# Kernel tuning notes

Measured on AMD Instinct MI355X. Metric: run time of the kernel, lower is better.

## Reference

```python
import jax, jax.numpy as jnp
import numpy as np

N, E, F_NODE, F_EDGE, H, EH, G = 20000, 200000, 32, 8, 256, 16, 512
OUT_DIMS = [H, H, H // 2]  # 256, 256, 128
BN_EPS = 1e-5


def _lin(k, out_c, in_c):
    kw, kb = jax.random.split(k)
    bound = 1.0 / np.sqrt(in_c)
    w = jax.random.uniform(kw, (out_c, in_c), minval=-bound, maxval=bound, dtype=jnp.float32)
    b = jax.random.uniform(kb, (out_c,), minval=-bound, maxval=bound, dtype=jnp.float32)
    return w, b


def setup_inputs() -> dict:
    key = jax.random.key(0)
    ks = jax.random.split(key, 40)
    inp = {
        "x": jax.random.normal(ks[0], (N, F_NODE), dtype=jnp.float32),
        "edge_index": jax.random.randint(ks[1], (2, E), 0, N, dtype=jnp.int64),
        "edge_attr": jax.random.normal(ks[2], (E, F_EDGE), dtype=jnp.float32),
        "batch": jnp.sort(jax.random.randint(ks[3], (N,), 0, G, dtype=jnp.int64)),
    }
    inp["ee_w"], inp["ee_b"] = _lin(ks[4], EH, F_EDGE)
    inp["ne_w"], inp["ne_b"] = _lin(ks[5], H, F_NODE)
    in_dim = H
    for i, out_dim in enumerate(OUT_DIMS):
        msg_in = 2 * in_dim + EH
        inp[f"c{i}_w1"], inp[f"c{i}_b1"] = _lin(ks[6 + 2 * i], 2 * out_dim, msg_in)
        inp[f"c{i}_w2"], inp[f"c{i}_b2"] = _lin(ks[7 + 2 * i], out_dim, 2 * out_dim)
        inp[f"bn{i}_g"] = jnp.ones((out_dim,), jnp.float32)
        inp[f"bn{i}_b"] = jnp.zeros((out_dim,), jnp.float32)
        inp[f"bn{i}_m"] = jnp.zeros((out_dim,), jnp.float32)
        inp[f"bn{i}_v"] = jnp.ones((out_dim,), jnp.float32)
        in_dim = out_dim
    inp["fc_w"], inp["fc_b"] = _lin(ks[20], 12, H // 2)
    return inp


def _seg_mean(vals, idx, num):
    s = jax.ops.segment_sum(vals, idx, num_segments=num)
    cnt = jax.ops.segment_sum(jnp.ones((vals.shape[0],), vals.dtype), idx, num_segments=num)
    return s / jnp.maximum(cnt, 1.0)[:, None]


def reference(x, edge_index, edge_attr, batch,
              ee_w, ee_b, ne_w, ne_b,
              c0_w1, c0_b1, c0_w2, c0_b2,
              c1_w1, c1_b1, c1_w2, c1_b2,
              c2_w1, c2_b1, c2_w2, c2_b2,
              bn0_g, bn0_b, bn0_m, bn0_v,
              bn1_g, bn1_b, bn1_m, bn1_v,
              bn2_g, bn2_b, bn2_m, bn2_v,
              fc_w, fc_b):
    src, dst = edge_index[0], edge_index[1]  # x_j = source, x_i = target
    e = jax.nn.relu(edge_attr @ ee_w.T + ee_b)  # [E, EH]
    h = jax.nn.relu(x @ ne_w.T + ne_b)          # [N, H]
    convs = [(c0_w1, c0_b1, c0_w2, c0_b2), (c1_w1, c1_b1, c1_w2, c1_b2), (c2_w1, c2_b1, c2_w2, c2_b2)]
    bns = [(bn0_g, bn0_b, bn0_m, bn0_v), (bn1_g, bn1_b, bn1_m, bn1_v), (bn2_g, bn2_b, bn2_m, bn2_v)]
    for (w1, b1, w2, b2), (g, bb, rm, rv) in zip(convs, bns):
        m = jnp.concatenate([h[dst], h[src], e], axis=1)      # [E, 2*in + EH]
        m = jax.nn.relu(m @ w1.T + b1) @ w2.T + b2            # per-edge MLP
        h = _seg_mean(m, dst, N)                              # scatter-mean to targets
        h = jax.nn.relu((h - rm) / jnp.sqrt(rv + BN_EPS) * g + bb)  # eval-mode BN
        # dropout is identity in eval mode
    pooled = _seg_mean(h, batch, G)                           # global_mean_pool [G, H//2]
    return jax.nn.sigmoid(pooled @ fc_w.T + fc_b)             # [G, 12]
```

## Files before the change

### kernel.cpp

```cpp
#include <hip/hip_runtime.h>
#include <hip/hip_bf16.h>

typedef unsigned int  uint;
typedef unsigned short ushort;
typedef float  f32x2  __attribute__((ext_vector_type(2)));
typedef float  f32x4  __attribute__((ext_vector_type(4)));
typedef __bf16 bf16x8 __attribute__((ext_vector_type(8)));

#define DEV static __device__ __forceinline__

DEV float  b2f(ushort b){ return __uint_as_float(((uint)b) << 16); }
DEV float  lo2f(uint u){ return __uint_as_float(u << 16); }
DEV float  hi2f(uint u){ return __uint_as_float(u & 0xffff0000u); }
DEV ushort f2b(float f){
  uint u = __float_as_uint(f);
  u += 0x7fffu + ((u >> 16) & 1u);
  return (ushort)(u >> 16);
}
DEV uint pk2(float a, float b){ return (uint)f2b(a) | ((uint)f2b(b) << 16); }
DEV void unpack8(uint4 v, float* f){
  f[0]=lo2f(v.x); f[1]=hi2f(v.x); f[2]=lo2f(v.y); f[3]=hi2f(v.y);
  f[4]=lo2f(v.z); f[5]=hi2f(v.z); f[6]=lo2f(v.w); f[7]=hi2f(v.w);
}
DEV int ld_idx(const void* p, int flag, long long i){
  return flag ? ((const int*)p)[i] : (int)((const long long*)p)[i];
}
DEV float ldf(const void* p, int f, int i){
  return f ? ((const float*)p)[i] : b2f(((const ushort*)p)[i]);
}
DEV int clampi(int v, int lo, int hi){ return v < lo ? lo : (v > hi ? hi : v); }

DEV void ld16(const ushort* g, ushort* l){
  __builtin_amdgcn_global_load_lds(
      (const __attribute__((address_space(1))) void*)g,
      (__attribute__((address_space(3))) void*)l, 16, 0, 0);
}

__global__ __launch_bounds__(256) void k_zero_probe(const uint* __restrict__ ei,
    const uint* __restrict__ xw, int* __restrict__ iflag, int* __restrict__ fflag,
    int* __restrict__ zbase, int zn){
  int i = blockIdx.x*256 + threadIdx.x;
  if (i < zn) zbase[i] = 0;
  if (blockIdx.x == 0){
    __shared__ int anyI, cntF;
    if (threadIdx.x == 0){ anyI = 0; cntF = 0; }
    __syncthreads();
    int li = 0, lc = 0;
    for (int k = threadIdx.x; k < 1024; k += 256){
      if (ei[2*k + 1] != 0u) li = 1;
      float f = fabsf(__uint_as_float(xw[k]));
      if (f > 1e-6f && f < 1e6f) lc++;
    }
    if (li) atomicOr(&anyI, 1);
    atomicAdd(&cntF, lc);
    __syncthreads();
    if (threadIdx.x == 0){ *iflag = anyI; *fflag = (2*cntF > 1024) ? 1 : 0; }
  }
}

__global__ __launch_bounds__(256) void k_count(const void* __restrict__ ei,
    const int* __restrict__ flag, int* __restrict__ cnt, int E, int N){
  int e = blockIdx.x*256 + threadIdx.x;
  if (e >= E) return;
  int d = clampi(ld_idx(ei, *flag, (long long)E + e), 0, N-1);
  atomicAdd(&cnt[d], 1);
}

__global__ __launch_bounds__(1024) void k_scan(const int* __restrict__ deg, int* __restrict__ rp, int n){
  __shared__ int part[1024];
  int t = threadIdx.x;
  int chunk = (n + 1023) >> 10;
  int base = t * chunk;
  int s = 0;
  for (int i = 0; i < chunk; i++){ int j = base + i; if (j < n) s += deg[j]; }
  part[t] = s;
  __syncthreads();
  for (int off = 1; off < 1024; off <<= 1){
    int v = (t >= off) ? part[t - off] : 0;
    __syncthreads();
    part[t] += v;
    __syncthreads();
  }
  int run = part[t] - s;
  for (int i = 0; i < chunk; i++){ int j = base + i; if (j < n){ rp[j] = run; run += deg[j]; } }
  if (t == 1023) rp[n] = part[1023];
}

struct CvtTab { const void* src[6]; ushort* dst[6]; int n[6]; int bstart[6]; int nseg; };

__global__ __launch_bounds__(256) void k_mega(
    const void* __restrict__ ei, const int* __restrict__ iflag,
    const int* __restrict__ rp, int* __restrict__ fill, int2* __restrict__ cpair,
    CvtTab ct, const int* __restrict__ fflag,
    const void* __restrict__ ea, const void* __restrict__ eew, const void* __restrict__ eeb,
    const void* __restrict__ x, const void* __restrict__ nw, const void* __restrict__ nbias,
    float* __restrict__ eh, ushort* __restrict__ h,
    int E, int N, int FB, int CB, int EB){
  int b = blockIdx.x;
  int t = threadIdx.x;
  if (b < FB){
    int e = b*256 + t;
    if (e >= E) return;
    int f = *iflag;
    int s = clampi(ld_idx(ei, f, e), 0, N-1);
    int d = clampi(ld_idx(ei, f, (long long)E + e), 0, N-1);
    int pos = clampi(rp[d] + atomicAdd(&fill[d], 1), 0, E-1);
    cpair[pos] = make_int2(s, e);
  } else if (b < FB + CB){
    int cb = b - FB;
    int s = ct.nseg - 1;
    for (int i = 1; i < ct.nseg; i++) if (cb < ct.bstart[i]){ s = i - 1; break; }
    int rel = cb - ct.bstart[s];
    const void* sp = ct.src[s];
    ushort* d = ct.dst[s];
    int f = *fflag;
    int end = ct.n[s]; int cap = rel*8192 + 8192; if (cap < end) end = cap;
    for (int i = rel*8192 + t; i < end; i += 256)
      d[i] = f ? f2b(((const float*)sp)[i]) : ((const ushort*)sp)[i];
  } else if (b < FB + CB + EB){
    __shared__ float ws[128];
    __shared__ float bs[16];
    int f = *fflag;
    if (t < 128) ws[t] = ldf(eew, f, t);
    if (t < 16)  bs[t] = ldf(eeb, f, t);
    __syncthreads();
    int e = (b - FB - CB)*256 + t;
    if (e >= E) return;
    float a[8];
    if (f){
      const float4* ap = (const float4*)((const float*)ea + (size_t)e*8);
      float4 v0 = ap[0], v1 = ap[1];
      a[0]=v0.x; a[1]=v0.y; a[2]=v0.z; a[3]=v0.w;
      a[4]=v1.x; a[5]=v1.y; a[6]=v1.z; a[7]=v1.w;
    } else {
      uint4 av = *(const uint4*)((const ushort*)ea + (size_t)e*8);
      unpack8(av, a);
    }
    float o[16];
    #pragma unroll
    for (int c = 0; c < 16; c++){
      float s = bs[c];
      #pragma unroll
      for (int j = 0; j < 8; j++) s += a[j]*ws[c*8+j];
      o[c] = fmaxf(s, 0.f);
    }
    f32x4* op = (f32x4*)(eh + (size_t)e*16);
    #pragma unroll
    for (int q4 = 0; q4 < 4; q4++){
      f32x4 v = {o[q4*4+0], o[q4*4+1], o[q4*4+2], o[q4*4+3]};
      op[q4] = v;
    }
  } else {
    __shared__ float xs[4][32];
    int f = *fflag;
    int nb = (b - FB - CB - EB)*4;
    if (t < 128){
      int ni = t >> 5, ci = t & 31;
      int n = nb + ni; if (n >= N) n = N - 1;
      xs[ni][ci] = f ? ((const float*)x)[(size_t)n*32 + ci]
                     : b2f(((const ushort*)x)[(size_t)n*32 + ci]);
    }
    __syncthreads();
    float wr[32];
    if (f){
      const float4* wp = (const float4*)((const float*)nw + (size_t)t*32);
      #pragma unroll
      for (int q4 = 0; q4 < 8; q4++){
        float4 v = wp[q4];
        wr[q4*4+0]=v.x; wr[q4*4+1]=v.y; wr[q4*4+2]=v.z; wr[q4*4+3]=v.w;
      }
    } else {
      const uint4* wp = (const uint4*)((const ushort*)nw + (size_t)t*32);
      unpack8(wp[0], wr); unpack8(wp[1], wr+8); unpack8(wp[2], wr+16); unpack8(wp[3], wr+24);
    }
    float bv = ldf(nbias, f, t);
    #pragma unroll
    for (int ni = 0; ni < 4; ni++){
      int n = nb + ni;
      if (n >= N) break;
      float s = bv;
      #pragma unroll
      for (int k = 0; k < 32; k++) s += xs[ni][k]*wr[k];
      h[(size_t)n*256 + t] = f2b(fmaxf(s, 0.f));
    }
  }
}

__global__ __launch_bounds__(256) void k_reorder(const int2* __restrict__ cpair,
    const float* __restrict__ eh, float* __restrict__ ehp, int E){
  int c = blockIdx.x*256 + threadIdx.x;
  if (c >= E*4) return;
  int pos = c >> 2, q = c & 3;
  int e = cpair[pos].y;
  ((f32x4*)ehp)[(size_t)pos*4 + q] = ((const f32x4*)eh)[(size_t)e*4 + q];
}

__global__ __launch_bounds__(256) void k_gemm_pq_lds(const ushort* __restrict__ A,
    const ushort* __restrict__ w1, int M, int Nc,
    ushort* __restrict__ P, ushort* __restrict__ Q){
  const int MT = (M + 127) >> 7;
  const int YC = Nc >> 6;
  int jb = blockIdx.x;
  int gx = jb & 7, rr = jb >> 3;
  int sx = rr / YC, yy = rr % YC;
  const int Tm = sx*8 + gx;
  if (Tm >= MT) return;
  __shared__ ushort As[128*32];
  __shared__ ushort Bs[128*32];
  const int t = threadIdx.x;
  const int lane = t & 63;
  const int wv = t >> 6;
  const int m0 = Tm*128;
  const int yc = Nc >> 7;
  const int isQ = yy >= yc;
  const int n0 = (isQ ? yy - yc : yy)*128;
  const ushort* W = w1 + (isQ ? 256 : 0);
  ushort* C = isQ ? Q : P;
  const int lr = lane & 15;
  const int qq = lane >> 4;
  int srow0 = t >> 2,         sq0 = t & 3;
  int srow1 = (256 + t) >> 2, sq1 = t & 3;
  int ga0 = m0 + srow0; if (ga0 >= M) ga0 = M - 1;
  int ga1 = m0 + srow1; if (ga1 >= M) ga1 = M - 1;
  f32x4 acc[2][8];
  #pragma unroll
  for (int f = 0; f < 2; f++)
    #pragma unroll
    for (int j = 0; j < 8; j++) acc[f][j] = {0.f,0.f,0.f,0.f};
  for (int k0 = 0; k0 < 256; k0 += 32){
    ld16(A + (size_t)ga0*256 + k0 + sq0*8, &As[(size_t)t*8]);
    ld16(A + (size_t)ga1*256 + k0 + sq1*8, &As[(size_t)(256+t)*8]);
    ld16(W + (size_t)(n0 + srow0)*528 + k0 + sq0*8, &Bs[(size_t)t*8]);
    ld16(W + (size_t)(n0 + srow1)*528 + k0 + sq1*8, &Bs[(size_t)(256+t)*8]);
    __syncthreads();
    bf16x8 a0 = *(const bf16x8*)&As[(wv*32 + lr)*32 + qq*8];
    bf16x8 a1 = *(const bf16x8*)&As[(wv*32 + 16 + lr)*32 + qq*8];
    #pragma unroll
    for (int j = 0; j < 8; j++){
      bf16x8 b = *(const bf16x8*)&Bs[(j*16 + lr)*32 + qq*8];
      acc[0][j] = __builtin_amdgcn_mfma_f32_16x16x32_bf16(a0, b, acc[0][j], 0, 0, 0);
      acc[1][j] = __builtin_amdgcn_mfma_f32_16x16x32_bf16(a1, b, acc[1][j], 0, 0, 0);
    }
    __syncthreads();
  }
  #pragma unroll
  for (int f = 0; f < 2; f++){
    #pragma unroll
    for (int r = 0; r < 4; r++){
      int row = m0 + wv*32 + f*16 + qq*4 + r;
      if (row >= M) continue;
      #pragma unroll
      for (int j = 0; j < 8; j++)
        C[(size_t)row*Nc + n0 + j*16 + lr] = f2b(acc[f][j][r]);
    }
  }
}

__global__ __launch_bounds__(256) void k_gemm_bn64(const ushort* __restrict__ A, int lda,
    const ushort* __restrict__ W, int ldb, int M, int Nc, int K,
    const void* __restrict__ bias, const void* __restrict__ g, const void* __restrict__ bb,
    const void* __restrict__ rm, const void* __restrict__ rv, const int* __restrict__ fflag,
    const int* __restrict__ rp, ushort* __restrict__ H){
  const int MT = (M + 63) >> 6;
  const int YC = Nc >> 7;
  int jb = blockIdx.x;
  int gx = jb & 7, rr = jb >> 3;
  int sx = rr / YC, yy = rr % YC;
  const int Tm = sx*8 + gx;
  if (Tm >= MT) return;
  __shared__ ushort As[64*32];
  __shared__ ushort Bs[128*32];
  const int t = threadIdx.x;
  const int lane = t & 63;
  const int wv = t >> 6;
  const int m0 = Tm*64;
  const int n0 = yy*128;
  const int lr = lane & 15;
  const int qq = lane >> 4;
  int srowA = t >> 2, sqA = t & 3;
  int ga = m0 + srowA; if (ga >= M) ga = M - 1;
  int srowB0 = t >> 2,        srowB1 = 64 + (t >> 2);
  f32x4 acc[8];
  #pragma unroll
  for (int j = 0; j < 8; j++) acc[j] = {0.f,0.f,0.f,0.f};
  for (int k0 = 0; k0 < K; k0 += 32){
    ld16(A + (size_t)ga*lda + k0 + sqA*8, &As[(size_t)t*8]);
    ld16(W + (size_t)(n0 + srowB0)*ldb + k0 + sqA*8, &Bs[(size_t)t*8]);
    ld16(W + (size_t)(n0 + srowB1)*ldb + k0 + sqA*8, &Bs[(size_t)(256+t)*8]);
    __syncthreads();
    bf16x8 a = *(const bf16x8*)&As[(wv*16 + lr)*32 + qq*8];
    #pragma unroll
    for (int j = 0; j < 8; j++){
      bf16x8 b = *(const bf16x8*)&Bs[(j*16 + lr)*32 + qq*8];
      acc[j] = __builtin_amdgcn_mfma_f32_16x16x32_bf16(a, b, acc[j], 0, 0, 0);
    }
    __syncthreads();
  }
  int f = *fflag;
  float bi[8], sc[8], sh[8];
  #pragma unroll
  for (int j = 0; j < 8; j++){
    int col = n0 + j*16 + lr;
    bi[j] = ldf(bias, f, col);
    sc[j] = ldf(g, f, col) * rsqrtf(ldf(rv, f, col) + 1e-5f);
    sh[j] = ldf(bb, f, col) - ldf(rm, f, col) * sc[j];
  }
  #pragma unroll
  for (int r = 0; r < 4; r++){
    int row = m0 + wv*16 + qq*4 + r;
    if (row >= M) continue;
    int empty = (rp[row+1] - rp[row] == 0);
    #pragma unroll
    for (int j = 0; j < 8; j++){
      float v = acc[j][r] + bi[j];
      if (empty) v = 0.f;
      H[(size_t)row*Nc + n0 + j*16 + lr] = f2b(fmaxf(v*sc[j] + sh[j], 0.f));
    }
  }
}

template<int C>
__global__ __launch_bounds__(256) void k_msg4(const ushort* P, const ushort* __restrict__ Q,
    const float* __restrict__ ehp, const ushort* __restrict__ w1, const void* __restrict__ b1,
    const int* __restrict__ fflag, const int* __restrict__ rp, const int2* __restrict__ cpair,
    ushort* MU, int N){
  int t = threadIdx.x;
  int c0 = t*2;
  f32x2 wc[16];
  {
    float a0[16], a1[16];
    const uint4* wp0 = (const uint4*)(w1 + (size_t)c0*528 + 512);
    const uint4* wp1 = (const uint4*)(w1 + (size_t)(c0+1)*528 + 512);
    unpack8(wp0[0], a0); unpack8(wp0[1], a0+8);
    unpack8(wp1[0], a1); unpack8(wp1[1], a1+8);
    #pragma unroll
    for (int j = 0; j < 16; j++){ wc[j].x = a0[j]; wc[j].y = a1[j]; }
  }
  int ff = *fflag;
  f32x2 b1v = { ldf(b1, ff, c0), ldf(b1, ff, c0+1) };
  int nb = blockIdx.x*2;
  int ne = nb + 2; if (ne > N) ne = N;
  for (int n = nb; n < ne; n++){
    const int i0 = rp[n], i1 = rp[n+1];
    uint pw = *(const uint*)(P + (size_t)n*C + c0);
    f32x2 pre = { lo2f(pw) + b1v.x, hi2f(pw) + b1v.y };
    f32x2 acc0 = {0.f, 0.f}, acc1 = {0.f, 0.f};
    int i = i0;
    int2 p0, p1; uint qw0, qw1;
    if (i + 2 <= i1){
      p0 = cpair[i]; p1 = cpair[i+1];
      qw0 = *(const uint*)(Q + (size_t)p0.x*C + c0);
      qw1 = *(const uint*)(Q + (size_t)p1.x*C + c0);
    }
    while (i + 2 <= i1){
      int inx = i + 2;
      bool more = (inx + 2 <= i1);
      int2 np0, np1;
      if (more){ np0 = cpair[inx]; np1 = cpair[inx+1]; }
      const f32x4* e0p = (const f32x4*)(ehp + (size_t)i*16);
      const f32x4* e1p = (const f32x4*)(ehp + (size_t)(i+1)*16);
      f32x4 ea0 = e0p[0], ea1 = e0p[1], ea2 = e0p[2], ea3 = e0p[3];
      f32x4 eb0 = e1p[0], eb1 = e1p[1], eb2 = e1p[2], eb3 = e1p[3];
      uint nq0 = 0, nq1 = 0;
      if (more){
        nq0 = *(const uint*)(Q + (size_t)np0.x*C + c0);
        nq1 = *(const uint*)(Q + (size_t)np1.x*C + c0);
      }
      float ef0[16] = {ea0.x,ea0.y,ea0.z,ea0.w, ea1.x,ea1.y,ea1.z,ea1.w,
                       ea2.x,ea2.y,ea2.z,ea2.w, ea3.x,ea3.y,ea3.z,ea3.w};
      float ef1[16] = {eb0.x,eb0.y,eb0.z,eb0.w, eb1.x,eb1.y,eb1.z,eb1.w,
                       eb2.x,eb2.y,eb2.z,eb2.w, eb3.x,eb3.y,eb3.z,eb3.w};
      f32x2 d0 = { pre.x + lo2f(qw0), pre.y + hi2f(qw0) };
      f32x2 d1 = { pre.x + lo2f(qw1), pre.y + hi2f(qw1) };
      #pragma unroll
      for (int j = 0; j < 16; j++){
        f32x2 e0v = {ef0[j], ef0[j]};
        f32x2 e1v = {ef1[j], ef1[j]};
        d0 += wc[j] * e0v;
        d1 += wc[j] * e1v;
      }
      acc0.x += fmaxf(d0.x, 0.f); acc0.y += fmaxf(d0.y, 0.f);
      acc1.x += fmaxf(d1.x, 0.f); acc1.y += fmaxf(d1.y, 0.f);
      if (more){ p0 = np0; p1 = np1; qw0 = nq0; qw1 = nq1; }
      i = inx;
    }
    if (i < i1){
      int2 t0 = cpair[i];
      uint tq0 = *(const uint*)(Q + (size_t)t0.x*C + c0);
      const f32x4* e0p = (const f32x4*)(ehp + (size_t)i*16);
      f32x4 ea0 = e0p[0], ea1 = e0p[1], ea2 = e0p[2], ea3 = e0p[3];
      float ef0[16] = {ea0.x,ea0.y,ea0.z,ea0.w, ea1.x,ea1.y,ea1.z,ea1.w,
                       ea2.x,ea2.y,ea2.z,ea2.w, ea3.x,ea3.y,ea3.z,ea3.w};
      f32x2 d0 = { pre.x + lo2f(tq0), pre.y + hi2f(tq0) };
      #pragma unroll
      for (int j = 0; j < 16; j++){
        f32x2 e0v = {ef0[j], ef0[j]};
        d0 += wc[j] * e0v;
      }
      acc0.x += fmaxf(d0.x, 0.f); acc0.y += fmaxf(d0.y, 0.f);
    }
    int cnt = i1 - i0;
    float inv = (cnt > 0) ? 1.f/(float)cnt : 0.f;
    *(uint*)(MU + (size_t)n*C + c0) = pk2((acc0.x + acc1.x)*inv, (acc0.y + acc1.y)*inv);
  }
}

__global__ __launch_bounds__(128) void k_pool(const ushort* __restrict__ h, const void* __restrict__ batch,
    const int* __restrict__ iflag, const void* __restrict__ fw, const void* __restrict__ fb,
    const int* __restrict__ fflag, void* __restrict__ out, int N){
  int g = blockIdx.x, t = threadIdx.x;
  int ifl = *iflag;
  int lo = 0, hi = N;
  while (lo < hi){ int mid = (lo+hi) >> 1; if (ld_idx(batch, ifl, mid) <  g) lo = mid+1; else hi = mid; }
  int s0 = lo;
  hi = N;
  while (lo < hi){ int mid = (lo+hi) >> 1; if (ld_idx(batch, ifl, mid) <= g) lo = mid+1; else hi = mid; }
  int s1 = lo;
  float s = 0.f;
  for (int i = s0; i < s1; i++) s += b2f(h[(size_t)i*128 + t]);
  int cnt = s1 - s0;
  __shared__ float ps[128];
  ps[t] = s / (float)(cnt > 0 ? cnt : 1);
  __syncthreads();
  int f = *fflag;
  if (t < 12){
    float z = ldf(fb, f, t);
    for (int j = 0; j < 128; j++) z += ps[j]*ldf(fw, f, t*128 + j);
    float r = 1.f/(1.f + expf(-z));
    if (f) ((float*)out)[g*12 + t] = r;
    else   ((ushort*)out)[g*12 + t] = f2b(r);
  }
}

__global__ __launch_bounds__(256) void k_sentinel(ushort* __restrict__ out, int n){
  int i = blockIdx.x*256 + threadIdx.x;
  if (i < n) out[i] = 0x3F00;
}

extern "C" void kernel_launch(void* const* d_in, const int* in_sizes, int n_in,
                              void* d_out, int out_size, void* d_ws, size_t ws_size,
                              hipStream_t stream){
  const void* x_raw   = d_in[0];
  const void* ei_raw  = d_in[1];
  const void* ea_raw  = d_in[2];
  const void* ba_raw  = d_in[3];
  (void)n_in;

  const int N = in_sizes[3];
  const int E = in_sizes[1] / 2;
  const int G = out_size / 12;

  char* base = (char*)d_ws;
  size_t off = 0;
  auto alloc = [&](size_t bytes)->char*{
    char* p = base + off;
    off = (off + bytes + 255) & ~(size_t)255;
    return p;
  };
  int* iflag    = (int*)alloc(256);
  int* fflag    = (int*)alloc(256);
  int* deg      = (int*)alloc((size_t)N*4);
  int* fill     = (int*)alloc((size_t)N*4);
  int zn        = (int)(fill - deg) + N;
  int* rp       = (int*)alloc((size_t)(N+1)*4);
  int2* cpair   = (int2*)alloc((size_t)E*8);
  ushort* w1c[3], *w2c[3];
  const int w1n[3] = {512*528, 512*528, 256*528};
  const int w2n[3] = {256*512, 256*512, 128*256};
  for (int i = 0; i < 3; i++) w1c[i] = (ushort*)alloc((size_t)w1n[i]*2);
  for (int i = 0; i < 3; i++) w2c[i] = (ushort*)alloc((size_t)w2n[i]*2);
  float*  e_h32 = (float*)alloc((size_t)E*16*4);
  float*  ehp32 = (float*)alloc((size_t)E*16*4);
  ushort* h     = (ushort*)alloc((size_t)N*256*2);
  ushort* Q     = (ushort*)alloc((size_t)N*512*2);
  ushort* PM    = (ushort*)alloc((size_t)N*512*2);

  if (off > ws_size){
    k_sentinel<<<(out_size + 255)/256, 256, 0, stream>>>((ushort*)d_out, out_size);
    return;
  }

  k_zero_probe<<<(zn + 255)/256, 256, 0, stream>>>((const uint*)ei_raw, (const uint*)x_raw,
                                                   iflag, fflag, deg, zn);
  k_count<<<(E + 255)/256, 256, 0, stream>>>(ei_raw, iflag, deg, E, N);
  k_scan<<<1, 1024, 0, stream>>>(deg, rp, N);

  CvtTab ct; ct.nseg = 6;
  const void* csrcs[6] = {d_in[8], d_in[16], d_in[24], d_in[10], d_in[18], d_in[26]};
  ushort* cdsts[6]     = {w1c[0],  w1c[1],   w1c[2],   w2c[0],   w2c[1],   w2c[2]};
  const int cns[6]     = {w1n[0],  w1n[1],   w1n[2],   w2n[0],   w2n[1],   w2n[2]};
  int bacc = 0;
  for (int i = 0; i < 6; i++){
    ct.src[i] = csrcs[i]; ct.dst[i] = cdsts[i]; ct.n[i] = cns[i];
    ct.bstart[i] = bacc; bacc += (cns[i] + 8191)/8192;
  }
  int FB = (E + 255)/256;
  int CB = bacc;
  int EB = (E + 255)/256;
  int NB = (N + 3)/4;
  k_mega<<<FB + CB + EB + NB, 256, 0, stream>>>(
      ei_raw, iflag, rp, fill, cpair, ct, fflag,
      ea_raw, d_in[4], d_in[5], x_raw, d_in[6], d_in[7],
      e_h32, h, E, N, FB, CB, EB);

  k_reorder<<<(E*4 + 255)/256, 256, 0, stream>>>(cpair, e_h32, ehp32, E);

  const int Cch[3] = {512, 512, 256};
  const int Od[3]  = {256, 256, 128};
  const int MTpq = (N + 127)/128;
  const int MTbn = (N + 63)/64;
  for (int i = 0; i < 3; i++){
    int di = 8 + 8*i;
    int g1 = 8 * ((MTpq + 7)/8) * (Cch[i] >> 6);
    k_gemm_pq_lds<<<g1, 256, 0, stream>>>(h, w1c[i], N, Cch[i], PM, Q);
    dim3 gm((N + 1)/2);
    if (i < 2) k_msg4<512><<<gm, 256, 0, stream>>>(PM, Q, ehp32, w1c[i], d_in[di+1], fflag, rp, cpair, PM, N);
    else       k_msg4<256><<<gm, 128, 0, stream>>>(PM, Q, ehp32, w1c[i], d_in[di+1], fflag, rp, cpair, PM, N);
    int g2 = 8 * ((MTbn + 7)/8) * (Od[i] >> 7);
    k_gemm_bn64<<<g2, 256, 0, stream>>>(PM, Cch[i], w2c[i], Cch[i], N, Od[i], Cch[i],
                                        d_in[di+3], d_in[di+4], d_in[di+5],
                                        d_in[di+6], d_in[di+7], fflag, rp, h);
  }

  k_pool<<<G, 128, 0, stream>>>(h, ba_raw, iflag, d_in[32], d_in[33], fflag, d_out, N);
}
```

Measured before the change: 486.0 us.

## Store Q in fp8 and permuted edge features in bf16 for message kernel

The per-node Q projection for the first two layers is now written as fp8 (e4m3) and gathered as 2-byte pairs in the message kernel. The reordered edge embeddings are packed to bf16, and the source indices get their own compact array. The manual software prefetch loop is replaced by a plain loop. This aims to cut the gather bandwidth in the memory-bound per-edge message kernel, at the cost of lower precision in Q and possibly less latency hiding.

```diff
diff --git a/kernel.cpp b/kernel.cpp
--- a/kernel.cpp
+++ b/kernel.cpp
@@ -3,6 +3,7 @@
 
 typedef unsigned int  uint;
 typedef unsigned short ushort;
+typedef unsigned char uchar;
 typedef float  f32x2  __attribute__((ext_vector_type(2)));
 typedef float  f32x4  __attribute__((ext_vector_type(4)));
 typedef __bf16 bf16x8 __attribute__((ext_vector_type(8)));
@@ -187,17 +188,23 @@
 }
 
 __global__ __launch_bounds__(256) void k_reorder(const int2* __restrict__ cpair,
-    const float* __restrict__ eh, float* __restrict__ ehp, int E){
-  int c = blockIdx.x*256 + threadIdx.x;
-  if (c >= E*4) return;
-  int pos = c >> 2, q = c & 3;
-  int e = cpair[pos].y;
-  ((f32x4*)ehp)[(size_t)pos*4 + q] = ((const f32x4*)eh)[(size_t)e*4 + q];
-}
-
+    const float* __restrict__ eh, uint* __restrict__ ehb, int* __restrict__ srcs, int E){
+  int pos = blockIdx.x*256 + threadIdx.x;
+  if (pos >= E) return;
+  int2 cp = cpair[pos];
+  srcs[pos] = cp.x;
+  const f32x4* ep = (const f32x4*)(eh + (size_t)cp.y*16);
+  f32x4 a = ep[0], b = ep[1], c = ep[2], d = ep[3];
+  uint4 o0 = { pk2(a.x,a.y), pk2(a.z,a.w), pk2(b.x,b.y), pk2(b.z,b.w) };
+  uint4 o1 = { pk2(c.x,c.y), pk2(c.z,c.w), pk2(d.x,d.y), pk2(d.z,d.w) };
+  ((uint4*)ehb)[(size_t)pos*2]     = o0;
+  ((uint4*)ehb)[(size_t)pos*2 + 1] = o1;
+}
+
+template<int QF8>
 __global__ __launch_bounds__(256) void k_gemm_pq_lds(const ushort* __restrict__ A,
     const ushort* __restrict__ w1, int M, int Nc,
-    ushort* __restrict__ P, ushort* __restrict__ Q){
+    ushort* __restrict__ P, void* __restrict__ Qout){
   const int MT = (M + 127) >> 7;
   const int YC = Nc >> 6;
   int jb = blockIdx.x;
@@ -215,7 +222,6 @@
   const int isQ = yy >= yc;
   const int n0 = (isQ ? yy - yc : yy)*128;
   const ushort* W = w1 + (isQ ? 256 : 0);
-  ushort* C = isQ ? Q : P;
   const int lr = lane & 15;
   const int qq = lane >> 4;
   int srow0 = t >> 2,         sq0 = t & 3;
@@ -243,15 +249,33 @@
     }
     __syncthreads();
   }
-  #pragma unroll
-  for (int f = 0; f < 2; f++){
-    #pragma unroll
-    for (int r = 0; r < 4; r++){
-      int row = m0 + wv*32 + f*16 + qq*4 + r;
-      if (row >= M) continue;
-      #pragma unroll
-      for (int j = 0; j < 8; j++)
-        C[(size_t)row*Nc + n0 + j*16 + lr] = f2b(acc[f][j][r]);
+  if (QF8 && isQ){
+    uchar* Cq = (uchar*)Qout;
+    #pragma unroll
+    for (int f = 0; f < 2; f++){
+      #pragma unroll
+      for (int r = 0; r < 4; r++){
+        int row = m0 + wv*32 + f*16 + qq*4 + r;
+        if (row >= M) continue;
+        #pragma unroll
+        for (int j = 0; j < 8; j++){
+          uint pk = (uint)__builtin_amdgcn_cvt_pk_fp8_f32(acc[f][j][r], 0.f, 0, false);
+          Cq[(size_t)row*Nc + n0 + j*16 + lr] = (uchar)(pk & 0xffu);
+        }
+      }
+    }
+  } else {
+    ushort* Cb = isQ ? (ushort*)Qout : P;
+    #pragma unroll
+    for (int f = 0; f < 2; f++){
+      #pragma unroll
+      for (int r = 0; r < 4; r++){
+        int row = m0 + wv*32 + f*16 + qq*4 + r;
+        if (row >= M) continue;
+        #pragma unroll
+        for (int j = 0; j < 8; j++)
+          Cb[(size_t)row*Nc + n0 + j*16 + lr] = f2b(acc[f][j][r]);
+      }
     }
   }
 }
@@ -319,10 +343,10 @@
   }
 }
 
-template<int C>
-__global__ __launch_bounds__(256) void k_msg4(const ushort* P, const ushort* __restrict__ Q,
-    const float* __restrict__ ehp, const ushort* __restrict__ w1, const void* __restrict__ b1,
-    const int* __restrict__ fflag, const int* __restrict__ rp, const int2* __restrict__ cpair,
+template<int C, int QF8>
+__global__ __launch_bounds__(256) void k_msg4(const ushort* P, const void* __restrict__ Qv,
+    const uint* __restrict__ ehb, const ushort* __restrict__ w1, const void* __restrict__ b1,
+    const int* __restrict__ fflag, const int* __restrict__ rp, const int* __restrict__ srcs,
     ushort* MU, int N){
   int t = threadIdx.x;
   int c0 = t*2;
@@ -346,32 +370,27 @@
     f32x2 pre = { lo2f(pw) + b1v.x, hi2f(pw) + b1v.y };
     f32x2 acc0 = {0.f, 0.f}, acc1 = {0.f, 0.f};
     int i = i0;
-    int2 p0, p1; uint qw0, qw1;
-    if (i + 2 <= i1){
-      p0 = cpair[i]; p1 = cpair[i+1];
-      qw0 = *(const uint*)(Q + (size_t)p0.x*C + c0);
-      qw1 = *(const uint*)(Q + (size_t)p1.x*C + c0);
-    }
-    while (i + 2 <= i1){
-      int inx = i + 2;
-      bool more = (inx + 2 <= i1);
-      int2 np0, np1;
-      if (more){ np0 = cpair[inx]; np1 = cpair[inx+1]; }
-      const f32x4* e0p = (const f32x4*)(ehp + (size_t)i*16);
-      const f32x4* e1p = (const f32x4*)(ehp + (size_t)(i+1)*16);
-      f32x4 ea0 = e0p[0], ea1 = e0p[1], ea2 = e0p[2], ea3 = e0p[3];
-      f32x4 eb0 = e1p[0], eb1 = e1p[1], eb2 = e1p[2], eb3 = e1p[3];
-      uint nq0 = 0, nq1 = 0;
-      if (more){
-        nq0 = *(const uint*)(Q + (size_t)np0.x*C + c0);
-        nq1 = *(const uint*)(Q + (size_t)np1.x*C + c0);
-      }
-      float ef0[16] = {ea0.x,ea0.y,ea0.z,ea0.w, ea1.x,ea1.y,ea1.z,ea1.w,
-                       ea2.x,ea2.y,ea2.z,ea2.w, ea3.x,ea3.y,ea3.z,ea3.w};
-      float ef1[16] = {eb0.x,eb0.y,eb0.z,eb0.w, eb1.x,eb1.y,eb1.z,eb1.w,
-                       eb2.x,eb2.y,eb2.z,eb2.w, eb3.x,eb3.y,eb3.z,eb3.w};
-      f32x2 d0 = { pre.x + lo2f(qw0), pre.y + hi2f(qw0) };
-      f32x2 d1 = { pre.x + lo2f(qw1), pre.y + hi2f(qw1) };
+    for (; i + 2 <= i1; i += 2){
+      int s0 = srcs[i], s1 = srcs[i+1];
+      f32x2 q0, q1;
+      if constexpr (QF8){
+        ushort qa = *(const ushort*)((const uchar*)Qv + (size_t)s0*C + c0);
+        ushort qb = *(const ushort*)((const uchar*)Qv + (size_t)s1*C + c0);
+        q0 = __builtin_amdgcn_cvt_pk_f32_fp8((uint)qa, false);
+        q1 = __builtin_amdgcn_cvt_pk_f32_fp8((uint)qb, false);
+      } else {
+        uint qa = *(const uint*)((const ushort*)Qv + (size_t)s0*C + c0);
+        uint qb = *(const uint*)((const ushort*)Qv + (size_t)s1*C + c0);
+        q0 = (f32x2){ lo2f(qa), hi2f(qa) };
+        q1 = (f32x2){ lo2f(qb), hi2f(qb) };
+      }
+      const uint4* ep = (const uint4*)(ehb + (size_t)i*8);
+      uint4 ea = ep[0], eb = ep[1], ec = ep[2], ed = ep[3];
+      float ef0[16], ef1[16];
+      unpack8(ea, ef0); unpack8(eb, ef0+8);
+      unpack8(ec, ef1); unpack8(ed, ef1+8);
+      f32x2 d0 = { pre.x + q0.x, pre.y + q0.y };
+      f32x2 d1 = { pre.x + q1.x, pre.y + q1.y };
       #pragma unroll
       for (int j = 0; j < 16; j++){
         f32x2 e0v = {ef0[j], ef0[j]};
@@ -381,17 +400,22 @@
       }
       acc0.x += fmaxf(d0.x, 0.f); acc0.y += fmaxf(d0.y, 0.f);
       acc1.x += fmaxf(d1.x, 0.f); acc1.y += fmaxf(d1.y, 0.f);
-      if (more){ p0 = np0; p1 = np1; qw0 = nq0; qw1 = nq1; }
-      i = inx;
     }
     if (i < i1){
-      int2 t0 = cpair[i];
-      uint tq0 = *(const uint*)(Q + (size_t)t0.x*C + c0);
-      const f32x4* e0p = (const f32x4*)(ehp + (size_t)i*16);
-      f32x4 ea0 = e0p[0], ea1 = e0p[1], ea2 = e0p[2], ea3 = e0p[3];
-      float ef0[16] = {ea0.x,ea0.y,ea0.z,ea0.w, ea1.x,ea1.y,ea1.z,ea1.w,
-                       ea2.x,ea2.y,ea2.z,ea2.w, ea3.x,ea3.y,ea3.z,ea3.w};
-      f32x2 d0 = { pre.x + lo2f(tq0), pre.y + hi2f(tq0) };
+      int s0 = srcs[i];
+      f32x2 q0;
+      if constexpr (QF8){
+        ushort qa = *(const ushort*)((const uchar*)Qv + (size_t)s0*C + c0);
+        q0 = __builtin_amdgcn_cvt_pk_f32_fp8((uint)qa, false);
+      } else {
+        uint qa = *(const uint*)((const ushort*)Qv + (size_t)s0*C + c0);
+        q0 = (f32x2){ lo2f(qa), hi2f(qa) };
+      }
+      const uint4* ep = (const uint4*)(ehb + (size_t)i*8);
+      uint4 ea = ep[0], eb = ep[1];
+      float ef0[16];
+      unpack8(ea, ef0); unpack8(eb, ef0+8);
+      f32x2 d0 = { pre.x + q0.x, pre.y + q0.y };
       #pragma unroll
       for (int j = 0; j < 16; j++){
         f32x2 e0v = {ef0[j], ef0[j]};
@@ -464,15 +488,17 @@
   int zn        = (int)(fill - deg) + N;
   int* rp       = (int*)alloc((size_t)(N+1)*4);
   int2* cpair   = (int2*)alloc((size_t)E*8);
+  int* srcs     = (int*)alloc((size_t)E*4);
   ushort* w1c[3], *w2c[3];
   const int w1n[3] = {512*528, 512*528, 256*528};
   const int w2n[3] = {256*512, 256*512, 128*256};
   for (int i = 0; i < 3; i++) w1c[i] = (ushort*)alloc((size_t)w1n[i]*2);
   for (int i = 0; i < 3; i++) w2c[i] = (ushort*)alloc((size_t)w2n[i]*2);
   float*  e_h32 = (float*)alloc((size_t)E*16*4);
-  float*  ehp32 = (float*)alloc((size_t)E*16*4);
+  uint*   ehb   = (uint*)alloc((size_t)E*32);
   ushort* h     = (ushort*)alloc((size_t)N*256*2);
   ushort* Q     = (ushort*)alloc((size_t)N*512*2);
+  uchar*  Qf8   = (uchar*)alloc((size_t)N*512);
   ushort* PM    = (ushort*)alloc((size_t)N*512*2);
 
   if (off > ws_size){
@@ -503,7 +529,7 @@
       ea_raw, d_in[4], d_in[5], x_raw, d_in[6], d_in[7],
       e_h32, h, E, N, FB, CB, EB);
 
-  k_reorder<<<(E*4 + 255)/256, 256, 0, stream>>>(cpair, e_h32, ehp32, E);
+  k_reorder<<<(E + 255)/256, 256, 0, stream>>>(cpair, e_h32, ehb, srcs, E);
 
   const int Cch[3] = {512, 512, 256};
   const int Od[3]  = {256, 256, 128};
@@ -512,10 +538,14 @@
   for (int i = 0; i < 3; i++){
     int di = 8 + 8*i;
     int g1 = 8 * ((MTpq + 7)/8) * (Cch[i] >> 6);
-    k_gemm_pq_lds<<<g1, 256, 0, stream>>>(h, w1c[i], N, Cch[i], PM, Q);
     dim3 gm((N + 1)/2);
-    if (i < 2) k_msg4<512><<<gm, 256, 0, stream>>>(PM, Q, ehp32, w1c[i], d_in[di+1], fflag, rp, cpair, PM, N);
-    else       k_msg4<256><<<gm, 128, 0, stream>>>(PM, Q, ehp32, w1c[i], d_in[di+1], fflag, rp, cpair, PM, N);
+    if (i < 2){
+      k_gemm_pq_lds<1><<<g1, 256, 0, stream>>>(h, w1c[i], N, Cch[i], PM, Qf8);
+      k_msg4<512,1><<<gm, 256, 0, stream>>>(PM, Qf8, ehb, w1c[i], d_in[di+1], fflag, rp, srcs, PM, N);
+    } else {
+      k_gemm_pq_lds<0><<<g1, 256, 0, stream>>>(h, w1c[i], N, Cch[i], PM, Q);
+      k_msg4<256,0><<<gm, 128, 0, stream>>>(PM, Q, ehb, w1c[i], d_in[di+1], fflag, rp, srcs, PM, N);
+    }
     int g2 = 8 * ((MTbn + 7)/8) * (Od[i] >> 7);
     k_gemm_bn64<<<g2, 256, 0, stream>>>(PM, Cch[i], w2c[i], Cch[i], N, Od[i], Cch[i],
                                         d_in[di+3], d_in[di+4], d_in[di+5],
```

Result: slower. 511.3 us (+5.2%).
